# Kernel tuning notes

Hardware: AMD Instinct MI355X
Metric: run time of the kernel (lower is better)

Reference implementation:

```python
import jax, jax.numpy as jnp
import numpy as np

N_NODES = 100000
N_EDGES = 3200000
D_IN = 128
D_HID = 16
N_CLS = 2


def gcn_conv(x, edge_index, W, b, n_nodes):
    """PyG GCNConv (normalize=True, add_self_loops=True, bias=True)."""
    h = x @ W  # [N, out]
    loop = jnp.arange(n_nodes, dtype=edge_index.dtype)
    src = jnp.concatenate([edge_index[0], loop])
    dst = jnp.concatenate([edge_index[1], loop])
    deg = jax.ops.segment_sum(jnp.ones_like(dst, dtype=h.dtype), dst, num_segments=n_nodes)
    dinv = jnp.where(deg > 0, jax.lax.rsqrt(deg), jnp.zeros_like(deg))
    norm = dinv[src] * dinv[dst]  # [E+N]
    msg = h[src] * norm[:, None]  # gather + scale
    out = jax.ops.segment_sum(msg, dst, num_segments=n_nodes)  # scatter-add
    return out + b


def setup_inputs() -> dict:
    key = jax.random.key(0)
    k1, k2, k3, k4, k5 = jax.random.split(key, 5)
    x = jax.random.normal(k1, (N_NODES, D_IN), dtype=jnp.float32)
    edge_index = jax.random.randint(k2, (2, N_EDGES), 0, N_NODES, dtype=jnp.int64)
    # Glorot-style init for GCNConv weights, zeros for bias (PyG default)
    W1 = jax.random.normal(k3, (D_IN, D_HID), dtype=jnp.float32) * (1.0 / np.sqrt(D_IN))
    b1 = jnp.zeros((D_HID,), dtype=jnp.float32)
    W2 = jax.random.normal(k4, (D_HID, N_CLS), dtype=jnp.float32) * (1.0 / np.sqrt(D_HID))
    b2 = jnp.zeros((N_CLS,), dtype=jnp.float32)
    return {"x": x, "edge_index": edge_index, "W1": W1, "b1": b1, "W2": W2, "b2": b2}


def reference(x, edge_index, W1, b1, W2, b2):
    n = x.shape[0]
    h = gcn_conv(x, edge_index, W1, b1, n)
    h = jax.nn.relu(h)
    # dropout is identity in eval mode
    h = gcn_conv(h, edge_index, W2, b2, n)
    return jax.nn.log_softmax(h, axis=1)
```

## Files before the change

kernel.cpp:

```cpp
#include <hip/hip_runtime.h>
#include <hip/hip_bf16.h>
#include <hip/hip_fp16.h>

#define D_IN  128
#define D_HID 16
#define N_CLS 2
#define NPB   256
#define MAXB  512
#define TILE  4096
#define XROW  136

#define FE 0

typedef short bf16x8 __attribute__((ext_vector_type(8)));
typedef float f32x4  __attribute__((ext_vector_type(4)));

__device__ __forceinline__ unsigned short f2bf(float f) {
    unsigned int u = __float_as_uint(f);
    u += 0x7FFFu + ((u >> 16) & 1u);
    return (unsigned short)(u >> 16);
}

template<bool I64>
__device__ __forceinline__ int lde(const void* p, size_t i) {
    if constexpr (I64) return (int)((const long long*)p)[i];
    else               return ((const int*)p)[i];
}

__global__ void k_detect(const int* __restrict__ ev, int* __restrict__ flags) {
    __shared__ int sE;
    if (threadIdx.x == 0) sE = 0;
    __syncthreads();
    if (ev[2 * threadIdx.x + 1] != 0) atomicOr(&sE, 1);
    __syncthreads();
    if (threadIdx.x == 0) flags[FE] = sE ? 0 : 1;
}

__global__ __launch_bounds__(MAXB) void k_init(const int* __restrict__ ev, int* __restrict__ flags,
                                               unsigned int* __restrict__ gcur, int cap) {
    __shared__ int sE;
    int tid = threadIdx.x;
    if (tid == 0) sE = 0;
    __syncthreads();
    if (tid < 256 && ev[2 * tid + 1] != 0) atomicOr(&sE, 1);
    gcur[tid] = (unsigned int)(tid * cap);
    __syncthreads();
    if (tid == 0) flags[FE] = sE ? 0 : 1;
}

template<bool I64>
__device__ __forceinline__ void part_body(
        const void* __restrict__ ei, unsigned int* __restrict__ gcur,
        unsigned int* __restrict__ staged, int E, int cap,
        unsigned int* sbuf, unsigned short* bbuf,
        int* hist, int* lbase, int* gb, int* wsum) {
    int tid = threadIdx.x;
    int t0 = blockIdx.x * TILE;

    hist[tid] = 0;
    __syncthreads();

    int myB[8]; unsigned int myP[8]; int myR[8];
#pragma unroll
    for (int k = 0; k < 8; ++k) {
        int e = t0 + k * 512 + tid;
        if (e < E) {
            int s = lde<I64>(ei, (size_t)e);
            int d = lde<I64>(ei, (size_t)E + e);
            int b = d >> 8;
            myB[k] = b;
            myP[k] = ((unsigned int)s << 8) | (unsigned int)(d & 255);
            myR[k] = atomicAdd(&hist[b], 1);
        } else myB[k] = -1;
    }
    __syncthreads();

    int v = hist[tid];
    int lane = tid & 63, wv = tid >> 6;
    int s = v;
#pragma unroll
    for (int m = 1; m < 64; m <<= 1) {
        int t = __shfl_up(s, m, 64);
        if (lane >= m) s += t;
    }
    if (lane == 63) wsum[wv] = s;
    __syncthreads();
    int woff = 0;
#pragma unroll
    for (int w = 0; w < 8; ++w) if (w < wv) woff += wsum[w];
    int excl = s + woff - v;
    lbase[tid] = excl;
    int gb_ = 0;
    if (v > 0) gb_ = (int)atomicAdd(&gcur[tid], (unsigned int)v);
    gb[tid] = gb_;
    __syncthreads();

#pragma unroll
    for (int k = 0; k < 8; ++k) {
        if (myB[k] >= 0) {
            int pos = lbase[myB[k]] + myR[k];
            sbuf[pos] = myP[k];
            bbuf[pos] = (unsigned short)myB[k];
        }
    }
    __syncthreads();

    int tot = lbase[MAXB - 1] + hist[MAXB - 1];
    for (int i = tid; i < tot; i += 512) {
        int b = bbuf[i];
        long long idx = (long long)gb[b] + (i - lbase[b]);
        if (idx < (long long)(b + 1) * cap)
            staged[idx] = sbuf[i];
    }
}

__global__ __launch_bounds__(512) void k_part(
        const void* __restrict__ ei, unsigned int* __restrict__ gcur,
        unsigned int* __restrict__ staged, int E, int cap, const int* __restrict__ flags) {
    __shared__ unsigned int sbuf[TILE];
    __shared__ unsigned short bbuf[TILE];
    __shared__ int hist[MAXB], lbase[MAXB], gb[MAXB];
    __shared__ int wsum[8];
    if (flags[FE]) part_body<true >(ei, gcur, staged, E, cap, sbuf, bbuf, hist, lbase, gb, wsum);
    else           part_body<false>(ei, gcur, staged, E, cap, sbuf, bbuf, hist, lbase, gb, wsum);
}

__global__ __launch_bounds__(512) void k_sortd(
        const unsigned int* __restrict__ staged, const unsigned int* __restrict__ gcur,
        unsigned int* __restrict__ staged2, unsigned int* __restrict__ dmeta,
        float* __restrict__ dinv, int cap, int N) {
    __shared__ unsigned int h[NPB];
    __shared__ unsigned int cur[NPB];
    __shared__ int wsum[4];
    int tid = threadIdx.x, b = blockIdx.x;
    long long s0 = (long long)b * cap;
    int cnt = (int)(gcur[b] - (unsigned int)s0);
    if (cnt > cap) cnt = cap;
    if (tid < NPB) h[tid] = 0u;
    __syncthreads();
    for (int i = tid; i < cnt; i += 512)
        atomicAdd(&h[staged[s0 + i] & 255], 1u);
    __syncthreads();
    int v = 0, sIncl = 0;
    int lane = tid & 63, wv = tid >> 6;
    if (tid < NPB) {
        v = (int)h[tid];
        sIncl = v;
#pragma unroll
        for (int m = 1; m < 64; m <<= 1) {
            int t = __shfl_up(sIncl, m, 64);
            if (lane >= m) sIncl += t;
        }
        if (lane == 63) wsum[wv] = sIncl;
    }
    __syncthreads();
    if (tid < NPB) {
        int woff = 0;
#pragma unroll
        for (int w = 0; w < 4; ++w) if (w < wv) woff += wsum[w];
        int excl = sIncl + woff - v;
        int node = b * NPB + tid;
        dmeta[node] = ((unsigned int)excl << 16) | (unsigned int)v;
        cur[tid] = (unsigned int)excl;
        if (node < N) dinv[node] = rsqrtf((float)(v + 1));
    }
    __syncthreads();
    for (int i = tid; i < cnt; i += 512) {
        unsigned int p = staged[s0 + i];
        unsigned int r = atomicAdd(&cur[p & 255], 1u);
        staged2[s0 + r] = p;
    }
}

__global__ __launch_bounds__(256) void k_gemm1m(
        const float* __restrict__ x, const float* __restrict__ W1,
        const float* __restrict__ dinv, __half* __restrict__ g1h, int n) {
    __shared__ short xhi[64 * XROW];
    __shared__ short xlo[64 * XROW];
    __shared__ short whi[16 * XROW];
    __shared__ short wlo[16 * XROW];
    int tid = threadIdx.x;
    int node0 = blockIdx.x * 64;

    for (int i = tid; i < D_IN * D_HID; i += 256) {
        int k = i >> 4, f = i & 15;
        float v = W1[i];
        unsigned short h = f2bf(v);
        float fh = __uint_as_float(((unsigned int)h) << 16);
        whi[f * XROW + k] = (short)h;
        wlo[f * XROW + k] = (short)f2bf(v - fh);
    }
    int limFlat = (n - node0) * D_IN;
#pragma unroll
    for (int it = 0; it < 8; ++it) {
        int flat = it * 1024 + tid * 4;
        float4 v = make_float4(0.f, 0.f, 0.f, 0.f);
        if (flat < limFlat) v = *(const float4*)(x + (size_t)node0 * D_IN + flat);
        int row = flat >> 7, k = flat & 127;
        unsigned short h0 = f2bf(v.x), h1 = f2bf(v.y), h2 = f2bf(v.z), h3 = f2bf(v.w);
        unsigned short l0 = f2bf(v.x - __uint_as_float(((unsigned int)h0) << 16));
        unsigned short l1 = f2bf(v.y - __uint_as_float(((unsigned int)h1) << 16));
        unsigned short l2 = f2bf(v.z - __uint_as_float(((unsigned int)h2) << 16));
        unsigned short l3 = f2bf(v.w - __uint_as_float(((unsigned int)h3) << 16));
        int o = row * XROW + k;
        *(uint2*)(&xhi[o]) = make_uint2((unsigned int)h0 | ((unsigned int)h1 << 16),
                                        (unsigned int)h2 | ((unsigned int)h3 << 16));
        *(uint2*)(&xlo[o]) = make_uint2((unsigned int)l0 | ((unsigned int)l1 << 16),
                                        (unsigned int)l2 | ((unsigned int)l3 << 16));
    }
    __syncthreads();

    int w = tid >> 6, L = tid & 63;
    int m = L & 15, q = L >> 4;
    const short* axh = &xhi[(w * 16 + m) * XROW + q * 8];
    const short* axl = &xlo[(w * 16 + m) * XROW + q * 8];
    const short* bwh = &whi[m * XROW + q * 8];
    const short* bwl = &wlo[m * XROW + q * 8];
    f32x4 acc = {0.f, 0.f, 0.f, 0.f};
#pragma unroll
    for (int c = 0; c < 4; ++c) {
        bf16x8 ah = *(const bf16x8*)(axh + c * 32);
        bf16x8 al = *(const bf16x8*)(axl + c * 32);
        bf16x8 bh = *(const bf16x8*)(bwh + c * 32);
        bf16x8 bl = *(const bf16x8*)(bwl + c * 32);
        acc = __builtin_amdgcn_mfma_f32_16x16x32_bf16(ah, bh, acc, 0, 0, 0);
        acc = __builtin_amdgcn_mfma_f32_16x16x32_bf16(ah, bl, acc, 0, 0, 0);
        acc = __builtin_amdgcn_mfma_f32_16x16x32_bf16(al, bh, acc, 0, 0, 0);
    }
    int nodeB = node0 + w * 16 + q * 4;
#pragma unroll
    for (int r = 0; r < 4; ++r) {
        int node = nodeB + r;
        if (node < n) g1h[(size_t)node * D_HID + m] = __float2half(dinv[node] * acc[r]);
    }
}

__global__ __launch_bounds__(1024) void k_agg1s(
        const unsigned int* __restrict__ staged2, const unsigned int* __restrict__ dmeta,
        const __half* __restrict__ g1h, const float* __restrict__ dinv,
        const float* __restrict__ b1, const float* __restrict__ W2,
        float2* __restrict__ g2, int N, int cap) {
    int tid = threadIdx.x, b = blockIdx.x;
    long long s0 = (long long)b * cap;
    int f2 = tid & 7;
    int dl = (tid >> 3) + (int)blockIdx.y * 128;
    int node = b * NPB + dl;
    unsigned int m = dmeta[b * NPB + dl];
    long long st = s0 + (m >> 16);
    int deg = (int)(m & 0xFFFFu);
    const __half2* g1h2 = (const __half2*)g1h;
    float ax = 0.f, ay = 0.f;
    for (int i = 0; i < deg; ++i) {
        unsigned int p = staged2[st + i];
        int src = (int)(p >> 8);
        float2 t = __half22float2(g1h2[(size_t)src * 8 + f2]);
        ax += t.x; ay += t.y;
    }
    float c0 = 0.f, c1 = 0.f, di = 0.f;
    if (node < N) {
        float2 t = __half22float2(g1h2[(size_t)node * 8 + f2]);
        ax += t.x; ay += t.y;
        di = dinv[node];
        int f0 = f2 * 2;
        float r0 = fmaxf(b1[f0] + di * ax, 0.f);
        float r1 = fmaxf(b1[f0 + 1] + di * ay, 0.f);
        c0 = r0 * W2[f0 * N_CLS + 0] + r1 * W2[(f0 + 1) * N_CLS + 0];
        c1 = r0 * W2[f0 * N_CLS + 1] + r1 * W2[(f0 + 1) * N_CLS + 1];
    }
#pragma unroll
    for (int mm = 1; mm <= 4; mm <<= 1) {
        c0 += __shfl_xor(c0, mm, 64);
        c1 += __shfl_xor(c1, mm, 64);
    }
    if (f2 == 0 && node < N) g2[node] = make_float2(di * c0, di * c1);
}

__global__ __launch_bounds__(1024) void k_agg2s(
        const unsigned int* __restrict__ staged2, const unsigned int* __restrict__ dmeta,
        const float2* __restrict__ g2, const float* __restrict__ dinv,
        const float* __restrict__ b2, float2* __restrict__ out, int N, int cap) {
    int tid = threadIdx.x, b = blockIdx.x;
    long long s0 = (long long)b * cap;
    int sl = tid & 3;
    int dl = tid >> 2;
    int node = b * NPB + dl;
    unsigned int m = dmeta[b * NPB + dl];
    long long st = s0 + (m >> 16);
    int deg = (int)(m & 0xFFFFu);
    float a0 = 0.f, a1 = 0.f;
    for (int i = sl; i < deg; i += 4) {
        unsigned int p = staged2[st + i];
        float2 t = g2[p >> 8];
        a0 += t.x; a1 += t.y;
    }
#pragma unroll
    for (int mm = 1; mm <= 2; mm <<= 1) {
        a0 += __shfl_xor(a0, mm, 64);
        a1 += __shfl_xor(a1, mm, 64);
    }
    if (sl == 0 && node < N) {
        float2 self = g2[node];
        float di = dinv[node];
        float v0 = b2[0] + di * (a0 + self.x);
        float v1 = b2[1] + di * (a1 + self.y);
        float mx = fmaxf(v0, v1);
        float lse = mx + logf(expf(v0 - mx) + expf(v1 - mx));
        out[node] = make_float2(v0 - lse, v1 - lse);
    }
}

__global__ void fb_deg_init(unsigned int* __restrict__ deg, int n) {
    int i = blockIdx.x * blockDim.x + threadIdx.x;
    if (i < n) deg[i] = 1u;
}
template<bool I64>
__global__ void fb_deg_count(const void* __restrict__ ei, unsigned int* __restrict__ deg,
                             int E, const int* __restrict__ flags) {
    if (flags[FE] != (int)I64) return;
    int e = blockIdx.x * blockDim.x + threadIdx.x;
    if (e < E) atomicAdd(&deg[lde<I64>(ei, (size_t)E + e)], 1u);
}
__global__ void fb_dinv_inplace(float* __restrict__ dinv, int n) {
    int i = blockIdx.x * blockDim.x + threadIdx.x;
    if (i < n) {
        unsigned int u = ((const unsigned int*)dinv)[i];
        dinv[i] = rsqrtf((float)u);
    }
}
__global__ void fb_a1_init(const float* __restrict__ h1, const float* __restrict__ dinv,
                           const float* __restrict__ b1, float* __restrict__ a1, int n) {
    int tid = blockIdx.x * blockDim.x + threadIdx.x;
    if (tid >= n * D_HID) return;
    int node = tid >> 4, f = tid & 15;
    float di = dinv[node];
    a1[tid] = b1[f] + di * di * h1[tid];
}
template<bool I64>
__global__ void fb_agg1(const void* __restrict__ ei, const float* __restrict__ dinv,
                        const float* __restrict__ h1, float* __restrict__ a1,
                        int E, const int* __restrict__ flags) {
    if (flags[FE] != (int)I64) return;
    int tid = blockIdx.x * blockDim.x + threadIdx.x;
    int e = tid >> 4, f = tid & 15;
    if (e >= E) return;
    int s = lde<I64>(ei, (size_t)e);
    int d = lde<I64>(ei, (size_t)E + e);
    float norm = dinv[s] * dinv[d];
    atomicAdd(&a1[(size_t)d * D_HID + f], h1[(size_t)s * D_HID + f] * norm);
}
__global__ void fb_relu_gemm2(const float* __restrict__ a1, const float* __restrict__ W2,
                              float* __restrict__ h2, int n) {
    int node = blockIdx.x * blockDim.x + threadIdx.x;
    if (node >= n) return;
    float c0 = 0.f, c1 = 0.f;
    const float* row = a1 + (size_t)node * D_HID;
#pragma unroll
    for (int f = 0; f < D_HID; ++f) {
        float r = fmaxf(row[f], 0.f);
        c0 += r * W2[f * N_CLS + 0];
        c1 += r * W2[f * N_CLS + 1];
    }
    h2[(size_t)node * 2 + 0] = c0;
    h2[(size_t)node * 2 + 1] = c1;
}
__global__ void fb_a2_init(const float* __restrict__ h2, const float* __restrict__ dinv,
                           const float* __restrict__ b2, float* __restrict__ a2, int n) {
    int tid = blockIdx.x * blockDim.x + threadIdx.x;
    if (tid >= n * N_CLS) return;
    int node = tid >> 1, c = tid & 1;
    float di = dinv[node];
    a2[tid] = b2[c] + di * di * h2[tid];
}
template<bool I64>
__global__ void fb_agg2(const void* __restrict__ ei, const float* __restrict__ dinv,
                        const float* __restrict__ h2, float* __restrict__ a2,
                        int E, const int* __restrict__ flags) {
    if (flags[FE] != (int)I64) return;
    int e = blockIdx.x * blockDim.x + threadIdx.x;
    if (e >= E) return;
    int s = lde<I64>(ei, (size_t)e);
    int d = lde<I64>(ei, (size_t)E + e);
    float norm = dinv[s] * dinv[d];
    atomicAdd(&a2[(size_t)d * 2 + 0], h2[(size_t)s * 2 + 0] * norm);
    atomicAdd(&a2[(size_t)d * 2 + 1], h2[(size_t)s * 2 + 1] * norm);
}
__global__ void fb_gemm1(const float* __restrict__ x, const float* __restrict__ W1,
                         float* __restrict__ h1, int n) {
    __shared__ float w[D_IN * D_HID];
    for (int i = threadIdx.x; i < D_IN * D_HID; i += blockDim.x) w[i] = W1[i];
    __syncthreads();
    int tid = blockIdx.x * blockDim.x + threadIdx.x;
    int node = tid >> 4, f = tid & 15;
    if (node >= n) return;
    const float4* xr = (const float4*)(x + (size_t)node * D_IN);
    float acc = 0.f;
#pragma unroll
    for (int k4 = 0; k4 < D_IN / 4; ++k4) {
        float4 v = xr[k4];
        int k = k4 * 4;
        acc += v.x * w[(k + 0) * D_HID + f];
        acc += v.y * w[(k + 1) * D_HID + f];
        acc += v.z * w[(k + 2) * D_HID + f];
        acc += v.w * w[(k + 3) * D_HID + f];
    }
    h1[tid] = acc;
}
__global__ void fb_lsm(const float* __restrict__ a2, float* __restrict__ out, int n) {
    int node = blockIdx.x * blockDim.x + threadIdx.x;
    if (node >= n) return;
    float v0 = a2[(size_t)node * 2 + 0];
    float v1 = a2[(size_t)node * 2 + 1];
    float m = fmaxf(v0, v1);
    float lse = m + logf(expf(v0 - m) + expf(v1 - m));
    out[(size_t)node * 2 + 0] = v0 - lse;
    out[(size_t)node * 2 + 1] = v1 - lse;
}

extern "C" void kernel_launch(void* const* d_in, const int* in_sizes, int n_in,
                              void* d_out, int out_size, void* d_ws, size_t ws_size,
                              hipStream_t stream) {
    const float* x  = (const float*)d_in[0];
    const void*  ei = d_in[1];
    const float* W1 = (const float*)d_in[2];
    const float* b1 = (const float*)d_in[3];
    const float* W2 = (const float*)d_in[4];
    const float* b2 = (const float*)d_in[5];

    const int N = in_sizes[0] / D_IN;
    const int E = in_sizes[1] / 2;
    const int nb = (N + NPB - 1) / NPB;

    int cap = ((2 * (E / nb + 1)) + 255) & ~255;
    if (cap < 1024) cap = 1024;

    const int B = 256;
    dim3 blk(B);
    const int nBlkN = (N + B - 1) / B;
    const int nBlkE = (E + B - 1) / B;
    char* ws = (char*)d_ws;

    auto al = [](size_t v) { return (v + 255) & ~(size_t)255; };
    const size_t oDinv   = 0;
    const size_t oDmeta  = al(oDinv + (size_t)N * 4);
    const size_t oGcur   = al(oDmeta + (size_t)nb * NPB * 4);
    const size_t oFlag   = al(oGcur + (size_t)MAXB * 4);
    const size_t oStage  = al(oFlag + 8);
    const size_t oStage2 = al(oStage + (size_t)nb * cap * 4);
    const size_t oG1h    = al(oStage2 + (size_t)nb * cap * 4);
    const size_t oG2     = al(oG1h + (size_t)N * D_HID * 2);
    const size_t needNew = al(oG2 + (size_t)N * 2 * 4);

    if (ws_size >= needNew && nb <= MAXB && cap <= 65280 && N < (1 << 24)) {
        float*        dinv    = (float*)(ws + oDinv);
        unsigned int* dmeta   = (unsigned int*)(ws + oDmeta);
        unsigned int* gcur    = (unsigned int*)(ws + oGcur);
        int*          flags   = (int*)(ws + oFlag);
        unsigned int* staged  = (unsigned int*)(ws + oStage);
        unsigned int* staged2 = (unsigned int*)(ws + oStage2);
        __half*       g1h     = (__half*)(ws + oG1h);
        float2*       g2      = (float2*)(ws + oG2);

        k_init<<<dim3(1), dim3(MAXB), 0, stream>>>((const int*)ei, flags, gcur, cap);

        dim3 gPart((E + TILE - 1) / TILE);
        k_part<<<gPart, dim3(512), 0, stream>>>(ei, gcur, staged, E, cap, flags);

        k_sortd<<<dim3(nb), dim3(512), 0, stream>>>(staged, gcur, staged2, dmeta, dinv, cap, N);

        k_gemm1m<<<dim3((N + 63) / 64), dim3(256), 0, stream>>>(x, W1, dinv, g1h, N);

        k_agg1s<<<dim3(nb, 2), dim3(1024), 0, stream>>>(staged2, dmeta, g1h, dinv, b1, W2, g2, N, cap);

        k_agg2s<<<dim3(nb), dim3(1024), 0, stream>>>(staged2, dmeta, g2, dinv, b2,
                                                     (float2*)d_out, N, cap);
    } else {
        float* dinv  = (float*)(ws + 0);
        float* h1    = (float*)(ws + 400128);
        float* a1    = (float*)(ws + 6800256);
        float* h2    = (float*)(ws + 13200384);
        float* a2    = (float*)(ws + 14000512);
        int*   flags = (int*)  (ws + 14800640);

        k_detect<<<dim3(1), blk, 0, stream>>>((const int*)ei, flags);
        fb_deg_init<<<dim3(nBlkN), blk, 0, stream>>>((unsigned int*)dinv, N);
        fb_deg_count<false><<<dim3(nBlkE), blk, 0, stream>>>(ei, (unsigned int*)dinv, E, flags);
        fb_deg_count<true ><<<dim3(nBlkE), blk, 0, stream>>>(ei, (unsigned int*)dinv, E, flags);
        fb_dinv_inplace<<<dim3(nBlkN), blk, 0, stream>>>(dinv, N);

        dim3 g_nh((N * D_HID + B - 1) / B);
        fb_gemm1<<<g_nh, blk, 0, stream>>>(x, W1, h1, N);
        fb_a1_init<<<g_nh, blk, 0, stream>>>(h1, dinv, b1, a1, N);
        dim3 g_eh(((size_t)E * D_HID + B - 1) / B);
        fb_agg1<false><<<g_eh, blk, 0, stream>>>(ei, dinv, h1, a1, E, flags);
        fb_agg1<true ><<<g_eh, blk, 0, stream>>>(ei, dinv, h1, a1, E, flags);
        fb_relu_gemm2<<<dim3(nBlkN), blk, 0, stream>>>(a1, W2, h2, N);
        dim3 g_n2((N * N_CLS + B - 1) / B);
        fb_a2_init<<<g_n2, blk, 0, stream>>>(h2, dinv, b2, a2, N);
        fb_agg2<false><<<dim3(nBlkE), blk, 0, stream>>>(ei, dinv, h2, a2, E, flags);
        fb_agg2<true ><<<dim3(nBlkE), blk, 0, stream>>>(ei, dinv, h2, a2, E, flags);
        fb_lsm<<<dim3(nBlkN), blk, 0, stream>>>(a2, (float*)d_out, N);
    }
}
```

Measured before the change: 238.5 us.

## Assign one wavefront per destination node in both aggregation kernels

Both CSR aggregation kernels switch from a few lanes per node to a whole 64-lane wavefront per node, looping each wave over 8 nodes of a 128-node slice. Layer 1 splits edges across 8 lane groups (8 feature pairs each) with a two-way unrolled gather, and layer 2 spreads edges across all 64 lanes, both ending in a shuffle reduction. The aim is more memory-level parallelism and better load balance per node, since average degree is about 32, in place of long serial per-thread edge loops. The cost is more shuffle reductions, idle lanes on low-degree nodes, and a sequential loop over nodes within each wave.

Result: no change. 240.2 us (+0.7%).

```diff
diff --git a/kernel.cpp b/kernel.cpp
--- a/kernel.cpp
+++ b/kernel.cpp
@@ -235,77 +235,93 @@
     }
 }
 
-__global__ __launch_bounds__(1024) void k_agg1s(
+__global__ __launch_bounds__(1024) void k_agg1w(
         const unsigned int* __restrict__ staged2, const unsigned int* __restrict__ dmeta,
         const __half* __restrict__ g1h, const float* __restrict__ dinv,
         const float* __restrict__ b1, const float* __restrict__ W2,
         float2* __restrict__ g2, int N, int cap) {
-    int tid = threadIdx.x, b = blockIdx.x;
+    int tid = threadIdx.x, b = blockIdx.x, by = blockIdx.y;
     long long s0 = (long long)b * cap;
-    int f2 = tid & 7;
-    int dl = (tid >> 3) + (int)blockIdx.y * 128;
-    int node = b * NPB + dl;
-    unsigned int m = dmeta[b * NPB + dl];
-    long long st = s0 + (m >> 16);
-    int deg = (int)(m & 0xFFFFu);
+    int wv = tid >> 6;
+    int lane = tid & 63;
+    int f2 = lane & 7;
+    int e8 = lane >> 3;
     const __half2* g1h2 = (const __half2*)g1h;
-    float ax = 0.f, ay = 0.f;
-    for (int i = 0; i < deg; ++i) {
-        unsigned int p = staged2[st + i];
-        int src = (int)(p >> 8);
-        float2 t = __half22float2(g1h2[(size_t)src * 8 + f2]);
-        ax += t.x; ay += t.y;
-    }
-    float c0 = 0.f, c1 = 0.f, di = 0.f;
-    if (node < N) {
-        float2 t = __half22float2(g1h2[(size_t)node * 8 + f2]);
-        ax += t.x; ay += t.y;
-        di = dinv[node];
-        int f0 = f2 * 2;
-        float r0 = fmaxf(b1[f0] + di * ax, 0.f);
-        float r1 = fmaxf(b1[f0 + 1] + di * ay, 0.f);
-        c0 = r0 * W2[f0 * N_CLS + 0] + r1 * W2[(f0 + 1) * N_CLS + 0];
-        c1 = r0 * W2[f0 * N_CLS + 1] + r1 * W2[(f0 + 1) * N_CLS + 1];
-    }
-#pragma unroll
-    for (int mm = 1; mm <= 4; mm <<= 1) {
-        c0 += __shfl_xor(c0, mm, 64);
-        c1 += __shfl_xor(c1, mm, 64);
-    }
-    if (f2 == 0 && node < N) g2[node] = make_float2(di * c0, di * c1);
-}
-
-__global__ __launch_bounds__(1024) void k_agg2s(
+    int dEnd = by * 128 + 128;
+    for (int dl = by * 128 + wv; dl < dEnd; dl += 16) {
+        int node = b * NPB + dl;
+        unsigned int m = dmeta[node];
+        long long st = s0 + (m >> 16);
+        int deg = (int)(m & 0xFFFFu);
+        float ax = 0.f, ay = 0.f;
+        int i = e8;
+        for (; i + 8 < deg; i += 16) {
+            unsigned int p0 = staged2[st + i];
+            unsigned int p1 = staged2[st + i + 8];
+            float2 t0 = __half22float2(g1h2[(size_t)(p0 >> 8) * 8 + f2]);
+            float2 t1 = __half22float2(g1h2[(size_t)(p1 >> 8) * 8 + f2]);
+            ax += t0.x + t1.x; ay += t0.y + t1.y;
+        }
+        if (i < deg) {
+            unsigned int p0 = staged2[st + i];
+            float2 t0 = __half22float2(g1h2[(size_t)(p0 >> 8) * 8 + f2]);
+            ax += t0.x; ay += t0.y;
+        }
+        ax += __shfl_xor(ax, 8, 64);  ay += __shfl_xor(ay, 8, 64);
+        ax += __shfl_xor(ax, 16, 64); ay += __shfl_xor(ay, 16, 64);
+        ax += __shfl_xor(ax, 32, 64); ay += __shfl_xor(ay, 32, 64);
+        float c0 = 0.f, c1 = 0.f, di = 0.f;
+        if (node < N) {
+            float2 t = __half22float2(g1h2[(size_t)node * 8 + f2]);
+            ax += t.x; ay += t.y;
+            di = dinv[node];
+            int f0 = f2 * 2;
+            float r0 = fmaxf(b1[f0] + di * ax, 0.f);
+            float r1 = fmaxf(b1[f0 + 1] + di * ay, 0.f);
+            c0 = r0 * W2[f0 * N_CLS + 0] + r1 * W2[(f0 + 1) * N_CLS + 0];
+            c1 = r0 * W2[f0 * N_CLS + 1] + r1 * W2[(f0 + 1) * N_CLS + 1];
+        }
+        c0 += __shfl_xor(c0, 1, 64); c1 += __shfl_xor(c1, 1, 64);
+        c0 += __shfl_xor(c0, 2, 64); c1 += __shfl_xor(c1, 2, 64);
+        c0 += __shfl_xor(c0, 4, 64); c1 += __shfl_xor(c1, 4, 64);
+        if (lane == 0 && node < N) g2[node] = make_float2(di * c0, di * c1);
+    }
+}
+
+__global__ __launch_bounds__(1024) void k_agg2w(
         const unsigned int* __restrict__ staged2, const unsigned int* __restrict__ dmeta,
         const float2* __restrict__ g2, const float* __restrict__ dinv,
         const float* __restrict__ b2, float2* __restrict__ out, int N, int cap) {
-    int tid = threadIdx.x, b = blockIdx.x;
+    int tid = threadIdx.x, b = blockIdx.x, by = blockIdx.y;
     long long s0 = (long long)b * cap;
-    int sl = tid & 3;
-    int dl = tid >> 2;
-    int node = b * NPB + dl;
-    unsigned int m = dmeta[b * NPB + dl];
-    long long st = s0 + (m >> 16);
-    int deg = (int)(m & 0xFFFFu);
-    float a0 = 0.f, a1 = 0.f;
-    for (int i = sl; i < deg; i += 4) {
-        unsigned int p = staged2[st + i];
-        float2 t = g2[p >> 8];
-        a0 += t.x; a1 += t.y;
-    }
-#pragma unroll
-    for (int mm = 1; mm <= 2; mm <<= 1) {
-        a0 += __shfl_xor(a0, mm, 64);
-        a1 += __shfl_xor(a1, mm, 64);
-    }
-    if (sl == 0 && node < N) {
-        float2 self = g2[node];
-        float di = dinv[node];
-        float v0 = b2[0] + di * (a0 + self.x);
-        float v1 = b2[1] + di * (a1 + self.y);
-        float mx = fmaxf(v0, v1);
-        float lse = mx + logf(expf(v0 - mx) + expf(v1 - mx));
-        out[node] = make_float2(v0 - lse, v1 - lse);
+    int wv = tid >> 6;
+    int lane = tid & 63;
+    int dEnd = by * 128 + 128;
+    for (int dl = by * 128 + wv; dl < dEnd; dl += 16) {
+        int node = b * NPB + dl;
+        unsigned int m = dmeta[node];
+        long long st = s0 + (m >> 16);
+        int deg = (int)(m & 0xFFFFu);
+        float a0 = 0.f, a1 = 0.f;
+        for (int i = lane; i < deg; i += 64) {
+            unsigned int p = staged2[st + i];
+            float2 t = g2[p >> 8];
+            a0 += t.x; a1 += t.y;
+        }
+#pragma unroll
+        for (int mm = 1; mm < 64; mm <<= 1) {
+            a0 += __shfl_xor(a0, mm, 64);
+            a1 += __shfl_xor(a1, mm, 64);
+        }
+        if (lane == 0 && node < N) {
+            float2 self = g2[node];
+            float di = dinv[node];
+            float v0 = b2[0] + di * (a0 + self.x);
+            float v1 = b2[1] + di * (a1 + self.y);
+            float mx = fmaxf(v0, v1);
+            float lse = mx + logf(expf(v0 - mx) + expf(v1 - mx));
+            out[node] = make_float2(v0 - lse, v1 - lse);
+        }
     }
 }
 
@@ -469,10 +485,10 @@
 
         k_gemm1m<<<dim3((N + 63) / 64), dim3(256), 0, stream>>>(x, W1, dinv, g1h, N);
 
-        k_agg1s<<<dim3(nb, 2), dim3(1024), 0, stream>>>(staged2, dmeta, g1h, dinv, b1, W2, g2, N, cap);
-
-        k_agg2s<<<dim3(nb), dim3(1024), 0, stream>>>(staged2, dmeta, g2, dinv, b2,
-                                                     (float2*)d_out, N, cap);
+        k_agg1w<<<dim3(nb, 2), dim3(1024), 0, stream>>>(staged2, dmeta, g1h, dinv, b1, W2, g2, N, cap);
+
+        k_agg2w<<<dim3(nb, 2), dim3(1024), 0, stream>>>(staged2, dmeta, g2, dinv, b2,
+                                                        (float2*)d_out, N, cap);
     } else {
         float* dinv  = (float*)(ws + 0);
         float* h1    = (float*)(ws + 400128);
```
